# Kernel optimization log

Hardware: AMD Instinct MI355X
Metric: run time of the kernel (lower is better)

## Reference

```python
import jax, jax.numpy as jnp
import numpy as np

K_FRAC = 0.5  # matches init kwarg k


def setup_inputs() -> dict:
    key = jax.random.key(0)
    g = jax.random.normal(key, (16, 2048, 2048), dtype=jnp.float32)
    return {"g": g}


def reference(g):
    # k = int(N * k_frac): number of SMALLEST entries per row to zero out
    N = g.shape[-1]
    k = int(N * K_FRAC)
    g2 = g.reshape(-1, N)                       # [R, N]
    # indices of the k smallest values per row (topk of -g)
    _, idx = jax.lax.top_k(-g2, k)              # [R, k] int32
    rows = jnp.arange(g2.shape[0])[:, None]     # [R, 1]
    t = g2.at[rows, idx].set(0.0)               # scatter zeros at bottom-k positions
    return t.reshape(g.shape)
```

## Files before the change

### kernel.cpp

```cpp
#include <hip/hip_runtime.h>

#define ROW_N 2048
#define ROW_K 1024

__device__ __forceinline__ unsigned f2key(float x) {
    unsigned u = __float_as_uint(x);
    return u ^ ((unsigned)((int)u >> 31) | 0x80000000u);
}

__global__ __launch_bounds__(256)
void ktakes_kernel(const float* __restrict__ g, float* __restrict__ out) {
    const int row = blockIdx.x;
    const int tid = threadIdx.x;
    const int wave = tid >> 6;
    const float* __restrict__ grow = g + (size_t)row * ROW_N;
    float* __restrict__ orow = out + (size_t)row * ROW_N;

    __shared__ unsigned hist4[4][256];
    __shared__ unsigned s_digit;
    __shared__ int s_rank;
    __shared__ int s_cnteq;
    __shared__ unsigned char s_flag[ROW_N];

    const float4* g4 = reinterpret_cast<const float4*>(grow);
    float4 va = g4[tid];
    float4 vb = g4[tid + 256];
    float xa[4] = {va.x, va.y, va.z, va.w};
    float xb[4] = {vb.x, vb.y, vb.z, vb.w};
    unsigned ka[4], kb[4];
#pragma unroll
    for (int c = 0; c < 4; ++c) { ka[c] = f2key(xa[c]); kb[c] = f2key(xb[c]); }

    unsigned prefix = 0;
    int rank = ROW_K - 1;

    for (int shift = 24; shift >= 0; shift -= 8) {
        unsigned* hflat = &hist4[0][0];
#pragma unroll
        for (int z = 0; z < 4; ++z) hflat[tid + 256 * z] = 0;
        __syncthreads();

        unsigned* h = hist4[wave];
        if (shift == 24) {
#pragma unroll
            for (int c = 0; c < 4; ++c) atomicAdd(&h[ka[c] >> 24], 1u);
#pragma unroll
            for (int c = 0; c < 4; ++c) atomicAdd(&h[kb[c] >> 24], 1u);
        } else {
            const unsigned hs = shift + 8;
#pragma unroll
            for (int c = 0; c < 4; ++c) {
                if (((ka[c] ^ prefix) >> hs) == 0)
                    atomicAdd(&h[(ka[c] >> shift) & 255u], 1u);
                if (((kb[c] ^ prefix) >> hs) == 0)
                    atomicAdd(&h[(kb[c] >> shift) & 255u], 1u);
            }
        }
        __syncthreads();

        if (tid < 64) {
            unsigned b[4];
#pragma unroll
            for (int j = 0; j < 4; ++j)
                b[j] = hist4[0][tid * 4 + j] + hist4[1][tid * 4 + j] +
                       hist4[2][tid * 4 + j] + hist4[3][tid * 4 + j];
            unsigned s = b[0] + b[1] + b[2] + b[3];
            unsigned incl = s;
#pragma unroll
            for (int off = 1; off < 64; off <<= 1) {
                unsigned n = __shfl_up(incl, off, 64);
                if (tid >= off) incl += n;
            }
            unsigned excl = incl - s;
            int r = rank;
            if (r >= (int)excl && r < (int)incl) {
                int rr = r - (int)excl;
                unsigned d = tid * 4;
                if (rr >= (int)b[0]) { rr -= (int)b[0]; d++;
                    if (rr >= (int)b[1]) { rr -= (int)b[1]; d++;
                        if (rr >= (int)b[2]) { rr -= (int)b[2]; d++; } } }
                s_digit = d;
                s_rank = rr;
            }
        }
        __syncthreads();
        prefix |= (s_digit << shift);
        rank = s_rank;
    }

    const unsigned Kth = prefix;
    const int m = rank + 1;

    if (tid == 0) s_cnteq = 0;
    __syncthreads();
    int eqc = 0;
#pragma unroll
    for (int c = 0; c < 4; ++c) eqc += (ka[c] == Kth) + (kb[c] == Kth);
    if (eqc) atomicAdd(&s_cnteq, eqc);
    __syncthreads();

    const bool simple = (s_cnteq == m);

    if (!simple) {
        if (tid == 0) {
            int cnt = 0;
            for (int i = 0; i < ROW_N; ++i) {
                unsigned u = f2key(grow[i]);
                unsigned char f = 0;
                if (u == Kth && cnt < m) { f = 1; cnt++; }
                s_flag[i] = f;
            }
        }
        __syncthreads();
    }

    float4 oa, ob;
    float ra[4], rb[4];
#pragma unroll
    for (int c = 0; c < 4; ++c) {
        bool za, zb;
        if (simple) {
            za = (ka[c] <= Kth);
            zb = (kb[c] <= Kth);
        } else {
            za = (ka[c] < Kth) || (ka[c] == Kth && s_flag[4 * tid + c]);
            zb = (kb[c] < Kth) || (kb[c] == Kth && s_flag[1024 + 4 * tid + c]);
        }
        ra[c] = za ? 0.0f : xa[c];
        rb[c] = zb ? 0.0f : xb[c];
    }
    oa.x = ra[0]; oa.y = ra[1]; oa.z = ra[2]; oa.w = ra[3];
    ob.x = rb[0]; ob.y = rb[1]; ob.z = rb[2]; ob.w = rb[3];

    float4* o4 = reinterpret_cast<float4*>(orow);
    o4[tid] = oa;
    o4[tid + 256] = ob;
}

extern "C" void kernel_launch(void* const* d_in, const int* in_sizes, int n_in,
                              void* d_out, int out_size, void* d_ws, size_t ws_size,
                              hipStream_t stream) {
    const float* g = (const float*)d_in[0];
    float* out = (float*)d_out;
    const int rows = in_sizes[0] / ROW_N;
    hipLaunchKernelGGL(ktakes_kernel, dim3(rows), dim3(256), 0, stream, g, out);
}
```

Baseline: 495.0 us.

## Assign one row per wavefront with wave-private histograms and ballot-based digit selection

```diff
diff --git a/kernel.cpp b/kernel.cpp
--- a/kernel.cpp
+++ b/kernel.cpp
@@ -2,139 +2,163 @@
 
 #define ROW_N 2048
 #define ROW_K 1024
+#define NSUB 4
+#define HPAD 264
+#define WH   (NSUB * HPAD)
+#define WSTRIDE (WH + 4)
+
+__device__ __forceinline__ void wfence() {
+    asm volatile("s_waitcnt lgkmcnt(0)" ::: "memory");
+}
 
 __device__ __forceinline__ unsigned f2key(float x) {
     unsigned u = __float_as_uint(x);
     return u ^ ((unsigned)((int)u >> 31) | 0x80000000u);
 }
+__device__ __forceinline__ float key2f(unsigned k) {
+    unsigned u = (k & 0x80000000u) ? (k ^ 0x80000000u) : ~k;
+    return __uint_as_float(u);
+}
 
 __global__ __launch_bounds__(256)
 void ktakes_kernel(const float* __restrict__ g, float* __restrict__ out) {
-    const int row = blockIdx.x;
-    const int tid = threadIdx.x;
+    const int tid  = threadIdx.x;
     const int wave = tid >> 6;
-    const float* __restrict__ grow = g + (size_t)row * ROW_N;
-    float* __restrict__ orow = out + (size_t)row * ROW_N;
+    const int lane = tid & 63;
+    const int row  = blockIdx.x * 4 + wave;
 
-    __shared__ unsigned hist4[4][256];
-    __shared__ unsigned s_digit;
-    __shared__ int s_rank;
-    __shared__ int s_cnteq;
-    __shared__ unsigned char s_flag[ROW_N];
+    __shared__ unsigned H[4 * WSTRIDE];
+    unsigned* hw   = H + wave * WSTRIDE;
+    unsigned* hsub = hw + (lane & (NSUB - 1)) * HPAD;
 
-    const float4* g4 = reinterpret_cast<const float4*>(grow);
-    float4 va = g4[tid];
-    float4 vb = g4[tid + 256];
-    float xa[4] = {va.x, va.y, va.z, va.w};
-    float xb[4] = {vb.x, vb.y, vb.z, vb.w};
-    unsigned ka[4], kb[4];
+    const float4* g4 = reinterpret_cast<const float4*>(g + (size_t)row * ROW_N);
+    float4*       o4 = reinterpret_cast<float4*>(out + (size_t)row * ROW_N);
+
+    unsigned k[32];
 #pragma unroll
-    for (int c = 0; c < 4; ++c) { ka[c] = f2key(xa[c]); kb[c] = f2key(xb[c]); }
+    for (int j = 0; j < 8; ++j) {
+        float4 v = g4[j * 64 + lane];
+        k[4*j+0] = f2key(v.x); k[4*j+1] = f2key(v.y);
+        k[4*j+2] = f2key(v.z); k[4*j+3] = f2key(v.w);
+    }
 
     unsigned prefix = 0;
     int rank = ROW_K - 1;
+    int cnteq = 0;
 
-    for (int shift = 24; shift >= 0; shift -= 8) {
-        unsigned* hflat = &hist4[0][0];
 #pragma unroll
-        for (int z = 0; z < 4; ++z) hflat[tid + 256 * z] = 0;
-        __syncthreads();
+    for (int r = 0; r < 4; ++r) {
+        const int shift = 24 - 8 * r;
 
-        unsigned* h = hist4[wave];
-        if (shift == 24) {
 #pragma unroll
-            for (int c = 0; c < 4; ++c) atomicAdd(&h[ka[c] >> 24], 1u);
+        for (int i = 0; i < 17; ++i) {
+            int idx = i * 64 + lane;
+            if (idx < WH) hw[idx] = 0;
+        }
+        wfence();
+
+        if (r == 0) {
 #pragma unroll
-            for (int c = 0; c < 4; ++c) atomicAdd(&h[kb[c] >> 24], 1u);
+            for (int c = 0; c < 32; ++c)
+                atomicAdd(&hsub[k[c] >> 24], 1u);
         } else {
-            const unsigned hs = shift + 8;
+            const int hs = shift + 8;
 #pragma unroll
-            for (int c = 0; c < 4; ++c) {
-                if (((ka[c] ^ prefix) >> hs) == 0)
-                    atomicAdd(&h[(ka[c] >> shift) & 255u], 1u);
-                if (((kb[c] ^ prefix) >> hs) == 0)
-                    atomicAdd(&h[(kb[c] >> shift) & 255u], 1u);
-            }
+            for (int c = 0; c < 32; ++c)
+                if (((k[c] ^ prefix) >> hs) == 0)
+                    atomicAdd(&hsub[(k[c] >> shift) & 255u], 1u);
         }
-        __syncthreads();
+        wfence();
 
-        if (tid < 64) {
-            unsigned b[4];
+        uint4 h0 = *reinterpret_cast<const uint4*>(&hw[0 * HPAD + 4 * lane]);
+        uint4 h1 = *reinterpret_cast<const uint4*>(&hw[1 * HPAD + 4 * lane]);
+        uint4 h2 = *reinterpret_cast<const uint4*>(&hw[2 * HPAD + 4 * lane]);
+        uint4 h3 = *reinterpret_cast<const uint4*>(&hw[3 * HPAD + 4 * lane]);
+        unsigned b0 = h0.x + h1.x + h2.x + h3.x;
+        unsigned b1 = h0.y + h1.y + h2.y + h3.y;
+        unsigned b2 = h0.z + h1.z + h2.z + h3.z;
+        unsigned b3 = h0.w + h1.w + h2.w + h3.w;
+        wfence();
+
+        unsigned s4 = b0 + b1 + b2 + b3;
+        unsigned incl = s4;
 #pragma unroll
-            for (int j = 0; j < 4; ++j)
-                b[j] = hist4[0][tid * 4 + j] + hist4[1][tid * 4 + j] +
-                       hist4[2][tid * 4 + j] + hist4[3][tid * 4 + j];
-            unsigned s = b[0] + b[1] + b[2] + b[3];
-            unsigned incl = s;
-#pragma unroll
-            for (int off = 1; off < 64; off <<= 1) {
-                unsigned n = __shfl_up(incl, off, 64);
-                if (tid >= off) incl += n;
-            }
-            unsigned excl = incl - s;
-            int r = rank;
-            if (r >= (int)excl && r < (int)incl) {
-                int rr = r - (int)excl;
-                unsigned d = tid * 4;
-                if (rr >= (int)b[0]) { rr -= (int)b[0]; d++;
-                    if (rr >= (int)b[1]) { rr -= (int)b[1]; d++;
-                        if (rr >= (int)b[2]) { rr -= (int)b[2]; d++; } } }
-                s_digit = d;
-                s_rank = rr;
-            }
+        for (int off = 1; off < 64; off <<= 1) {
+            unsigned n = __shfl_up(incl, off, 64);
+            if (lane >= off) incl += n;
         }
-        __syncthreads();
-        prefix |= (s_digit << shift);
-        rank = s_rank;
+        int excl = (int)(incl - s4);
+        bool found = (rank >= excl) && (rank < (int)incl);
+
+        int rr = rank - excl;
+        unsigned d = 4 * lane;
+        unsigned beq = b0;
+        if (found) {
+            if (rr >= (int)b0) { rr -= (int)b0; d++; beq = b1;
+                if (rr >= (int)b1) { rr -= (int)b1; d++; beq = b2;
+                    if (rr >= (int)b2) { rr -= (int)b2; d++; beq = b3; } } }
+        }
+        unsigned long long bal = __ballot(found);
+        int src = __builtin_ctzll(bal);
+        d     = (unsigned)__shfl((int)d, src, 64);
+        rr    = __shfl(rr, src, 64);
+        beq   = (unsigned)__shfl((int)beq, src, 64);
+
+        prefix |= d << shift;
+        rank  = rr;
+        cnteq = (int)beq;
     }
 
     const unsigned Kth = prefix;
     const int m = rank + 1;
 
-    if (tid == 0) s_cnteq = 0;
-    __syncthreads();
-    int eqc = 0;
+    unsigned zm = 0;
+    if (cnteq == m) {
 #pragma unroll
-    for (int c = 0; c < 4; ++c) eqc += (ka[c] == Kth) + (kb[c] == Kth);
-    if (eqc) atomicAdd(&s_cnteq, eqc);
-    __syncthreads();
-
-    const bool simple = (s_cnteq == m);
-
-    if (!simple) {
-        if (tid == 0) {
-            int cnt = 0;
-            for (int i = 0; i < ROW_N; ++i) {
-                unsigned u = f2key(grow[i]);
-                unsigned char f = 0;
-                if (u == Kth && cnt < m) { f = 1; cnt++; }
-                s_flag[i] = f;
+        for (int c = 0; c < 32; ++c)
+            if (k[c] <= Kth) zm |= 1u << c;
+    } else {
+        int base = 0;
+#pragma unroll
+        for (int j = 0; j < 8; ++j) {
+            int eqmask = 0, e = 0;
+#pragma unroll
+            for (int c = 0; c < 4; ++c) {
+                bool q = (k[4*j+c] == Kth);
+                eqmask |= (int)q << c; e += (int)q;
             }
+            int incl = e;
+#pragma unroll
+            for (int off = 1; off < 64; off <<= 1) {
+                int n = __shfl_up(incl, off, 64);
+                if (lane >= off) incl += n;
+            }
+            int excl = incl - e;
+            int tot = __shfl(incl, 63, 64);
+            int pos = base + excl;
+#pragma unroll
+            for (int c = 0; c < 4; ++c) {
+                if (eqmask & (1 << c)) {
+                    if (pos < m) zm |= 1u << (4*j+c);
+                    pos++;
+                }
+            }
+            base += tot;
         }
-        __syncthreads();
+#pragma unroll
+        for (int c = 0; c < 32; ++c)
+            if (k[c] < Kth) zm |= 1u << c;
     }
 
-    float4 oa, ob;
-    float ra[4], rb[4];
 #pragma unroll
-    for (int c = 0; c < 4; ++c) {
-        bool za, zb;
-        if (simple) {
-            za = (ka[c] <= Kth);
-            zb = (kb[c] <= Kth);
-        } else {
-            za = (ka[c] < Kth) || (ka[c] == Kth && s_flag[4 * tid + c]);
-            zb = (kb[c] < Kth) || (kb[c] == Kth && s_flag[1024 + 4 * tid + c]);
-        }
-        ra[c] = za ? 0.0f : xa[c];
-        rb[c] = zb ? 0.0f : xb[c];
+    for (int j = 0; j < 8; ++j) {
+        float4 v;
+        v.x = (zm >> (4*j+0)) & 1u ? 0.0f : key2f(k[4*j+0]);
+        v.y = (zm >> (4*j+1)) & 1u ? 0.0f : key2f(k[4*j+1]);
+        v.z = (zm >> (4*j+2)) & 1u ? 0.0f : key2f(k[4*j+2]);
+        v.w = (zm >> (4*j+3)) & 1u ? 0.0f : key2f(k[4*j+3]);
+        o4[j * 64 + lane] = v;
     }
-    oa.x = ra[0]; oa.y = ra[1]; oa.z = ra[2]; oa.w = ra[3];
-    ob.x = rb[0]; ob.y = rb[1]; ob.z = rb[2]; ob.w = rb[3];
-
-    float4* o4 = reinterpret_cast<float4*>(orow);
-    o4[tid] = oa;
-    o4[tid + 256] = ob;
 }
 
 extern "C" void kernel_launch(void* const* d_in, const int* in_sizes, int n_in,
@@ -143,5 +167,5 @@
     const float* g = (const float*)d_in[0];
     float* out = (float*)d_out;
     const int rows = in_sizes[0] / ROW_N;
-    hipLaunchKernelGGL(ktakes_kernel, dim3(rows), dim3(256), 0, stream, g, out);
+    hipLaunchKernelGGL(ktakes_kernel, dim3(rows / 4), dim3(256), 0, stream, g, out);
 }
```

After: 433.0 us. 12.5% less time.
